# Kernel optimization log

Hardware: AMD Instinct MI355X
Metric: run time of the kernel (lower is better)

## Reference

```python
import jax, jax.numpy as jnp
import numpy as np

NUM_LAYERS = 2
D = 1024          # d_model
H = 16            # nhead
HD = D // H       # head_dim = 64
FF = 4096         # dim_feedforward
S, N, L = 1024, 2, 4096
EPS = 1e-5


def _layer_norm(x, g, b):
    mu = jnp.mean(x, axis=-1, keepdims=True)
    var = jnp.var(x, axis=-1, keepdims=True)
    return (x - mu) * jax.lax.rsqrt(var + EPS) * g + b


def setup_inputs() -> dict:
    key = jax.random.key(0)
    ks = jax.random.split(key, 16)
    w = 0.02
    return {
        "key_in": jax.random.normal(ks[0], (S, N, D), jnp.float32),
        "value_in": jax.random.normal(ks[1], (S, N, D), jnp.float32),
        "query": jax.random.normal(ks[2], (L, N, D), jnp.float32),
        "in_proj_w": jax.random.normal(ks[3], (NUM_LAYERS, 3 * D, D), jnp.float32) * w,
        "in_proj_b": jnp.zeros((NUM_LAYERS, 3 * D), jnp.float32),
        "out_w": jax.random.normal(ks[4], (NUM_LAYERS, D, D), jnp.float32) * w,
        "out_b": jnp.zeros((NUM_LAYERS, D), jnp.float32),
        "ln1_g": jnp.ones((NUM_LAYERS, D), jnp.float32),
        "ln1_b": jnp.zeros((NUM_LAYERS, D), jnp.float32),
        "ln2_g": jnp.ones((NUM_LAYERS, D), jnp.float32),
        "ln2_b": jnp.zeros((NUM_LAYERS, D), jnp.float32),
        "ff1_w": jax.random.normal(ks[5], (NUM_LAYERS, FF, D), jnp.float32) * w,
        "ff1_b": jnp.zeros((NUM_LAYERS, FF), jnp.float32),
        "ff2_w": jax.random.normal(ks[6], (NUM_LAYERS, D, FF), jnp.float32) * w,
        "ff2_b": jnp.zeros((NUM_LAYERS, D), jnp.float32),
    }


def reference(key_in, value_in, query, in_proj_w, in_proj_b, out_w, out_b,
              ln1_g, ln1_b, ln2_g, ln2_b, ff1_w, ff1_b, ff2_w, ff2_b):
    scaling = float(HD) ** -0.5
    noise_key = jax.random.key(42)
    tgt = query
    attn_map = None
    for i in range(NUM_LAYERS):
        Wq, Wk, Wv = in_proj_w[i, :D], in_proj_w[i, D:2 * D], in_proj_w[i, 2 * D:]
        bq, bk, bv = in_proj_b[i, :D], in_proj_b[i, D:2 * D], in_proj_b[i, 2 * D:]
        q = (tgt @ Wq.T + bq) * scaling              # [L,N,D]
        k = key_in @ Wk.T + bk                       # [S,N,D]
        v = value_in @ Wv.T + bv                     # [S,N,D]
        qh = q.reshape(L, N, H, HD).transpose(1, 2, 0, 3)   # [N,H,L,HD]
        kh = k.reshape(S, N, H, HD).transpose(1, 2, 0, 3)   # [N,H,S,HD]
        vh = v.reshape(S, N, H, HD).transpose(1, 2, 0, 3)   # [N,H,S,HD]
        scores = jnp.einsum('nhld,nhsd->nhls', qh, kh)      # [N,H,L,S]
        # add_noise_term: zero logit column + random value token
        scores = jnp.concatenate(
            [scores, jnp.zeros((N, H, L, 1), scores.dtype)], axis=-1)
        noise = jax.random.normal(jax.random.fold_in(noise_key, i),
                                  (N, H, 1, HD), vh.dtype)
        vh = jnp.concatenate([vh, noise], axis=2)           # [N,H,S+1,HD]
        w = jax.nn.softmax(scores, axis=-1)                 # [N,H,L,S+1]
        seg = jax.nn.sigmoid(w)                             # sigmoid of softmax
        out = jnp.einsum('nhls,nhsd->nhld', w, vh)          # [N,H,L,HD]
        out = out.transpose(2, 0, 1, 3).reshape(L, N, D)
        out = out @ out_w[i].T + out_b[i]
        attn_map = seg.mean(axis=1)[:, :, :-1]              # [N,L,S], noise col dropped
        x = _layer_norm(tgt + out, ln1_g[i], ln1_b[i])
        h = jax.nn.relu(x @ ff1_w[i].T + ff1_b[i]) @ ff2_w[i].T + ff2_b[i]
        tgt = _layer_norm(x + h, ln2_g[i], ln2_b[i])
    return tgt, attn_map
```

## Files before the change

kernel.cpp:

```cpp
#include <hip/hip_runtime.h>
#include <hip/hip_bf16.h>


typedef __bf16 bf16x8 __attribute__((ext_vector_type(8)));
typedef float  f32x4  __attribute__((ext_vector_type(4)));

__device__ __forceinline__ f32x4 mfma16(bf16x8 a, bf16x8 b, f32x4 c) {
    return __builtin_amdgcn_mfma_f32_16x16x32_bf16(a, b, c, 0, 0, 0);
}

__device__ __forceinline__ void load_lds16(const __bf16* g, __bf16* l) {
    __builtin_amdgcn_global_load_lds(
        (const __attribute__((address_space(1))) void*)g,
        (__attribute__((address_space(3))) void*)l, 16, 0, 0);
}

__device__ __forceinline__ int swz8(int o, int nwg) {
    return (o & 7) * (nwg >> 3) + (o >> 3);
}

__global__ __launch_bounds__(256) void cast_k(const float* __restrict__ in,
                                              __bf16* __restrict__ out, int n4) {
    int i = blockIdx.x * 256 + threadIdx.x;
    if (i >= n4) return;
    float4 f = ((const float4*)in)[i];
    union { uint2 u; __bf16 h[4]; } ob;
    ob.h[0] = (__bf16)f.x; ob.h[1] = (__bf16)f.y;
    ob.h[2] = (__bf16)f.z; ob.h[3] = (__bf16)f.w;
    ((uint2*)out)[i] = ob.u;
}

__global__ __launch_bounds__(512, 2) void gemm8p(
    const __bf16* __restrict__ A, const __bf16* __restrict__ B,
    const float* __restrict__ bias, __bf16* __restrict__ C,
    int N, int K, float scale, int relu)
{
    __shared__ __bf16 L[8][8192];
    const int tid = threadIdx.x;
    const int wid = tid >> 6, lane = tid & 63;
    const int lq = lane >> 4, lc = lane & 15;
    const int wm = wid >> 2;
    const int wn = (wid & 3) * 64;
    const int bh = wn >> 7;
    const int lb = wn & 127;
    const int sw = lc & 7;
    const int w = swz8(blockIdx.x, gridDim.x);
    const int nt = N >> 8;
    const int bm = (w / nt) * 256, bn = (w % nt) * 256;
    const int NT = K >> 6;

    auto stageA = [&](int kt, int h) {
#pragma unroll
        for (int p = 0; p < 2; ++p) {
            const int cc = p * 512 + tid;
            const int row = cc >> 3, gk = ((cc & 7) ^ (row & 7)) * 8;
            load_lds16(A + (size_t)(bm + h * 128 + row) * K + (kt * 64 + gk),
                       &L[(kt & 1) * 4 + h][(size_t)cc * 8]);
        }
    };
    auto stageB = [&](int kt, int h) {
#pragma unroll
        for (int p = 0; p < 2; ++p) {
            const int cc = p * 512 + tid;
            const int row = cc >> 3, gk = ((cc & 7) ^ (row & 7)) * 8;
            load_lds16(B + (size_t)(bn + h * 128 + row) * K + (kt * 64 + gk),
                       &L[(kt & 1) * 4 + 2 + h][(size_t)cc * 8]);
        }
    };

    stageA(0, 0); stageA(0, 1); stageB(0, 0); stageB(0, 1);
    stageA(1, 0); stageA(1, 1); stageB(1, 0); stageB(1, 1);
    asm volatile("s_waitcnt vmcnt(8)" ::: "memory");
    __builtin_amdgcn_s_barrier();
    __builtin_amdgcn_sched_barrier(0);

    const f32x4 fz = {0.f, 0.f, 0.f, 0.f};
    f32x4 acc[2][4][4];
#pragma unroll
    for (int rh = 0; rh < 2; ++rh)
#pragma unroll
        for (int i = 0; i < 4; ++i)
#pragma unroll
            for (int jj = 0; jj < 4; ++jj) acc[rh][i][jj] = fz;

    for (int t = 0; t < NT; ++t) {
        const __bf16* __restrict__ Ah = &L[(t & 1) * 4 + wm][0];
        const __bf16* __restrict__ Bh = &L[(t & 1) * 4 + 2 + bh][0];
        const int pf = (t + 2 < NT);
        bf16x8 a[2][4], b0[2][2], b1[2][2];

#pragma unroll
        for (int kk = 0; kk < 2; ++kk) {
            const int sl = ((kk * 4 + lq) ^ sw) * 8;
#pragma unroll
            for (int i = 0; i < 4; ++i)
                a[kk][i] = *(const bf16x8*)&Ah[(i * 16 + lc) * 64 + sl];
#pragma unroll
            for (int j = 0; j < 2; ++j)
                b0[kk][j] = *(const bf16x8*)&Bh[(lb + j * 16 + lc) * 64 + sl];
        }
        __builtin_amdgcn_s_barrier();
        asm volatile("s_waitcnt lgkmcnt(0)" ::: "memory");
        __builtin_amdgcn_sched_barrier(0);
        __builtin_amdgcn_s_setprio(1);
#pragma unroll
        for (int kk = 0; kk < 2; ++kk)
#pragma unroll
            for (int i = 0; i < 4; ++i)
#pragma unroll
                for (int j = 0; j < 2; ++j)
                    acc[0][i][j] = mfma16(a[kk][i], b0[kk][j], acc[0][i][j]);
        __builtin_amdgcn_s_setprio(0);
        __builtin_amdgcn_s_barrier();
        __builtin_amdgcn_sched_barrier(0);

#pragma unroll
        for (int kk = 0; kk < 2; ++kk) {
            const int sl = ((kk * 4 + lq) ^ sw) * 8;
#pragma unroll
            for (int j = 0; j < 2; ++j)
                b1[kk][j] = *(const bf16x8*)&Bh[(lb + 32 + j * 16 + lc) * 64 + sl];
        }
        __builtin_amdgcn_s_barrier();
        asm volatile("s_waitcnt lgkmcnt(0)" ::: "memory");
        __builtin_amdgcn_sched_barrier(0);
        __builtin_amdgcn_s_setprio(1);
#pragma unroll
        for (int kk = 0; kk < 2; ++kk)
#pragma unroll
            for (int i = 0; i < 4; ++i)
#pragma unroll
                for (int j = 0; j < 2; ++j)
                    acc[0][i][2 + j] = mfma16(a[kk][i], b1[kk][j], acc[0][i][2 + j]);
        __builtin_amdgcn_s_setprio(0);
        __builtin_amdgcn_s_barrier();
        __builtin_amdgcn_sched_barrier(0);

#pragma unroll
        for (int kk = 0; kk < 2; ++kk) {
            const int sl = ((kk * 4 + lq) ^ sw) * 8;
#pragma unroll
            for (int i = 0; i < 4; ++i)
                a[kk][i] = *(const bf16x8*)&Ah[(64 + i * 16 + lc) * 64 + sl];
        }
        if (pf) { stageB(t + 2, 0); stageB(t + 2, 1); }
        __builtin_amdgcn_s_barrier();
        asm volatile("s_waitcnt lgkmcnt(0)" ::: "memory");
        __builtin_amdgcn_sched_barrier(0);
        __builtin_amdgcn_s_setprio(1);
#pragma unroll
        for (int kk = 0; kk < 2; ++kk)
#pragma unroll
            for (int i = 0; i < 4; ++i)
#pragma unroll
                for (int j = 0; j < 2; ++j)
                    acc[1][i][j] = mfma16(a[kk][i], b0[kk][j], acc[1][i][j]);
        __builtin_amdgcn_s_setprio(0);
        __builtin_amdgcn_s_barrier();
        __builtin_amdgcn_sched_barrier(0);

        if (pf) { stageA(t + 2, 0); stageA(t + 2, 1); }
        __builtin_amdgcn_s_barrier();
        __builtin_amdgcn_sched_barrier(0);
        __builtin_amdgcn_s_setprio(1);
#pragma unroll
        for (int kk = 0; kk < 2; ++kk)
#pragma unroll
            for (int i = 0; i < 4; ++i)
#pragma unroll
                for (int j = 0; j < 2; ++j)
                    acc[1][i][2 + j] = mfma16(a[kk][i], b1[kk][j], acc[1][i][2 + j]);
        __builtin_amdgcn_s_setprio(0);
        if (pf) asm volatile("s_waitcnt vmcnt(8)" ::: "memory");
        else    asm volatile("s_waitcnt vmcnt(0)" ::: "memory");
        __builtin_amdgcn_s_barrier();
        __builtin_amdgcn_sched_barrier(0);
    }

    float bv[4];
#pragma unroll
    for (int q = 0; q < 4; ++q) bv[q] = bias[bn + wn + q * 16 + lc];
#pragma unroll
    for (int rh = 0; rh < 2; ++rh)
#pragma unroll
        for (int i = 0; i < 4; ++i)
#pragma unroll
            for (int r = 0; r < 4; ++r) {
                const int row = bm + wm * 128 + rh * 64 + i * 16 + lq * 4 + r;
                const size_t base = (size_t)row * N + bn + wn + lc;
#pragma unroll
                for (int ch = 0; ch < 2; ++ch)
#pragma unroll
                    for (int j = 0; j < 2; ++j) {
                        float v = (acc[rh][i][ch * 2 + j][r] + bv[ch * 2 + j]) * scale;
                        if (relu) v = fmaxf(v, 0.f);
                        C[base + ch * 32 + j * 16] = (__bf16)v;
                    }
            }
}

__global__ __launch_bounds__(512, 2) void gemm8pN(
    const __bf16* __restrict__ A, const __bf16* __restrict__ B,
    const float* __restrict__ bias, __bf16* __restrict__ C,
    int N, int K, float scale, int relu)
{
    __shared__ __bf16 L[6][8192];
    const int tid = threadIdx.x;
    const int wid = tid >> 6, lane = tid & 63;
    const int lq = lane >> 4, lc = lane & 15;
    const int wr = (wid >> 1) * 64;
    const int wc = (wid & 1) * 64;
    const int ha = wr >> 7;
    const int lr = wr & 127;
    const int sw = lc & 7;
    const int w = swz8(blockIdx.x, gridDim.x);
    const int nt = N >> 7;
    const int bm = (w / nt) * 256, bn = (w % nt) * 128;
    const int NT = K >> 6;

    auto stageA = [&](int kt, int h) {
#pragma unroll
        for (int p = 0; p < 2; ++p) {
            const int cc = p * 512 + tid;
            const int row = cc >> 3, gk = ((cc & 7) ^ (row & 7)) * 8;
            load_lds16(A + (size_t)(bm + h * 128 + row) * K + (kt * 64 + gk),
                       &L[(kt & 1) * 3 + h][(size_t)cc * 8]);
        }
    };
    auto stageB = [&](int kt) {
#pragma unroll
        for (int p = 0; p < 2; ++p) {
            const int cc = p * 512 + tid;
            const int row = cc >> 3, gk = ((cc & 7) ^ (row & 7)) * 8;
            load_lds16(B + (size_t)(bn + row) * K + (kt * 64 + gk),
                       &L[(kt & 1) * 3 + 2][(size_t)cc * 8]);
        }
    };

    stageA(0, 0); stageA(0, 1); stageB(0);
    stageA(1, 0); stageA(1, 1); stageB(1);
    asm volatile("s_waitcnt vmcnt(6)" ::: "memory");
    __builtin_amdgcn_s_barrier();
    __builtin_amdgcn_sched_barrier(0);

    const f32x4 fz = {0.f, 0.f, 0.f, 0.f};
    f32x4 acc[4][4];
#pragma unroll
    for (int i = 0; i < 4; ++i)
#pragma unroll
        for (int j = 0; j < 4; ++j) acc[i][j] = fz;

    for (int t = 0; t < NT; ++t) {
        const __bf16* __restrict__ Ah = &L[(t & 1) * 3 + ha][0];
        const __bf16* __restrict__ Bb = &L[(t & 1) * 3 + 2][0];
        const int pf = (t + 2 < NT);
        bf16x8 a[2][4], b[2][4];

#pragma unroll
        for (int kk = 0; kk < 2; ++kk) {
            const int sl = ((kk * 4 + lq) ^ sw) * 8;
#pragma unroll
            for (int i = 0; i < 4; ++i)
                a[kk][i] = *(const bf16x8*)&Ah[(lr + i * 16 + lc) * 64 + sl];
#pragma unroll
            for (int j = 0; j < 4; ++j)
                b[kk][j] = *(const bf16x8*)&Bb[(wc + j * 16 + lc) * 64 + sl];
        }
        __builtin_amdgcn_s_barrier();
        asm volatile("s_waitcnt lgkmcnt(0)" ::: "memory");
        __builtin_amdgcn_sched_barrier(0);
        __builtin_amdgcn_s_setprio(1);
#pragma unroll
        for (int i = 0; i < 4; ++i)
#pragma unroll
            for (int j = 0; j < 4; ++j)
                acc[i][j] = mfma16(a[0][i], b[0][j], acc[i][j]);
        __builtin_amdgcn_s_setprio(0);
        __builtin_amdgcn_s_barrier();
        __builtin_amdgcn_sched_barrier(0);

        if (pf) { stageB(t + 2); stageA(t + 2, 0); stageA(t + 2, 1); }
        __builtin_amdgcn_s_setprio(1);
#pragma unroll
        for (int i = 0; i < 4; ++i)
#pragma unroll
            for (int j = 0; j < 4; ++j)
                acc[i][j] = mfma16(a[1][i], b[1][j], acc[i][j]);
        __builtin_amdgcn_s_setprio(0);
        if (pf) asm volatile("s_waitcnt vmcnt(6)" ::: "memory");
        else    asm volatile("s_waitcnt vmcnt(0)" ::: "memory");
        __builtin_amdgcn_s_barrier();
        __builtin_amdgcn_sched_barrier(0);
    }

    float bv[4];
#pragma unroll
    for (int q = 0; q < 4; ++q) bv[q] = bias[bn + wc + q * 16 + lc];
#pragma unroll
    for (int i = 0; i < 4; ++i)
#pragma unroll
        for (int r = 0; r < 4; ++r) {
            const int row = bm + wr + i * 16 + lq * 4 + r;
            const size_t base = (size_t)row * N + bn + wc + lc;
#pragma unroll
            for (int j = 0; j < 4; ++j) {
                float v = (acc[i][j][r] + bv[j]) * scale;
                if (relu) v = fmaxf(v, 0.f);
                C[base + j * 16] = (__bf16)v;
            }
        }
}

template <int BN>
__device__ __forceinline__ void gemm_core(
    const __bf16* __restrict__ A, const __bf16* __restrict__ B,
    const float* __restrict__ bias, __bf16* __restrict__ C,
    int M, int N, int K, float scale, int relu, int bm, int bn,
    __bf16* As, __bf16* Bs)
{
    const int tid = threadIdx.x;
    const int wave = tid >> 6, lane = tid & 63;
    const int lq = lane >> 4, lc = lane & 15;
    const int WN = BN / 2;
    const int JT = WN / 16;
    const int wm = (wave >> 1) * 64, wn = (wave & 1) * WN;

    const f32x4 fz = {0.f, 0.f, 0.f, 0.f};
    f32x4 acc[4][4];
#pragma unroll
    for (int i = 0; i < 4; ++i)
#pragma unroll
        for (int j = 0; j < JT; ++j) acc[i][j] = fz;

    const int sw = lc & 7;

    for (int k0 = 0; k0 < K; k0 += 64) {
        __syncthreads();
#pragma unroll
        for (int i = 0; i < 4; ++i) {
            const int c = tid + 256 * i;
            const int row = c >> 3, gk = ((c & 7) ^ (row & 7)) * 8;
            load_lds16(A + (size_t)(bm + row) * K + (k0 + gk),
                       As + (size_t)c * 8);
        }
#pragma unroll
        for (int i = 0; i < BN / 32; ++i) {
            const int c = tid + 256 * i;
            const int row = c >> 3, gk = ((c & 7) ^ (row & 7)) * 8;
            load_lds16(B + (size_t)(bn + row) * K + (k0 + gk),
                       Bs + (size_t)c * 8);
        }
        __syncthreads();
#pragma unroll
        for (int kk = 0; kk < 2; ++kk) {
            bf16x8 af[4], bw[4];
            const int slot = ((kk * 4 + lq) ^ sw) * 8;
#pragma unroll
            for (int i = 0; i < 4; ++i)
                af[i] = *(const bf16x8*)&As[(wm + i * 16 + lc) * 64 + slot];
#pragma unroll
            for (int j = 0; j < JT; ++j)
                bw[j] = *(const bf16x8*)&Bs[(wn + j * 16 + lc) * 64 + slot];
#pragma unroll
            for (int i = 0; i < 4; ++i)
#pragma unroll
                for (int j = 0; j < JT; ++j)
                    acc[i][j] = mfma16(af[i], bw[j], acc[i][j]);
        }
    }

#pragma unroll
    for (int j = 0; j < JT; ++j) {
        const int col = bn + wn + j * 16 + lc;
        const float bv = bias[col];
#pragma unroll
        for (int i = 0; i < 4; ++i) {
#pragma unroll
            for (int r = 0; r < 4; ++r) {
                float v = (acc[i][j][r] + bv) * scale;
                if (relu) v = fmaxf(v, 0.f);
                const int row = bm + wm + i * 16 + lq * 4 + r;
                C[(size_t)row * N + col] = (__bf16)v;
            }
        }
    }
}

__global__ __launch_bounds__(256) void gemm_qkv(
    const __bf16* __restrict__ TGT, const __bf16* __restrict__ KIN,
    const __bf16* __restrict__ VIN, const __bf16* __restrict__ W,
    const float* __restrict__ bias, __bf16* __restrict__ PROJ,
    __bf16* __restrict__ KB, __bf16* __restrict__ VB)
{
    __shared__ __bf16 As[128 * 64];
    __shared__ __bf16 Bs[64 * 64];
    const int bid = swz8(blockIdx.x, 1536);
    const __bf16* A; __bf16* Cout; int M, t, seg; float scale;
    if (bid < 1024)      { seg = 0; t = bid;        A = TGT; Cout = PROJ; M = 8192; scale = 0.125f; }
    else if (bid < 1280) { seg = 1; t = bid - 1024; A = KIN; Cout = KB;   M = 2048; scale = 1.f; }
    else                 { seg = 2; t = bid - 1280; A = VIN; Cout = VB;   M = 2048; scale = 1.f; }
    gemm_core<64>(A, W + (size_t)seg * 1048576, bias + seg * 1024, Cout,
                  M, 1024, 1024, scale, 0, (t >> 4) * 128, (t & 15) * 64, As, Bs);
}

__global__ __launch_bounds__(256) void transpose_v(const __bf16* __restrict__ v,
                                                   __bf16* __restrict__ vt) {
    __shared__ __bf16 t[64][72];
    const int tid = threadIdx.x;
    const int s0 = blockIdx.x * 64, h = blockIdx.y, n = blockIdx.z;
#pragma unroll
    for (int i = 0; i < 2; ++i) {
        const int cc = tid + 256 * i, row = cc >> 3, kc = (cc & 7) * 8;
        *(uint4*)&t[row][kc] =
            *(const uint4*)(v + ((size_t)((s0 + row) * 2 + n)) * 1024 + h * 64 + kc);
    }
    __syncthreads();
#pragma unroll
    for (int i = 0; i < 2; ++i) {
        const int cc = tid + 256 * i, d = cc >> 3, jc = (cc & 7) * 8;
        __attribute__((aligned(16))) __bf16 tmp[8];
#pragma unroll
        for (int u = 0; u < 8; ++u) tmp[u] = t[jc + u][d];
        *(uint4*)(vt + ((size_t)((n * 16 + h) * 64 + d)) * 1024 + s0 + jc) = *(uint4*)tmp;
    }
}

__global__ __launch_bounds__(256) void attn_fused(
    const __bf16* __restrict__ q, const __bf16* __restrict__ kk,
    const __bf16* __restrict__ vt, float* __restrict__ cvec,
    __bf16* __restrict__ aout)
{
    __shared__ __bf16 qs[64][72];
    __shared__ __bf16 ks[64][72];
    __shared__ __bf16 vs[64][72];
    __shared__ __bf16 es[64][72];
    const int tid = threadIdx.x, wave = tid >> 6, lane = tid & 63;
    const int lq = lane >> 4, lc = lane & 15;
    const int o = (blockIdx.z * 16 + blockIdx.y) * 64 + blockIdx.x;
    const int w = swz8(o, 2048);
    const int l0 = (w & 63) * 64, h = (w >> 6) & 15, n = w >> 10;
    const int wr = wave * 16;
#pragma unroll
    for (int i = 0; i < 2; ++i) {
        const int cc = tid + 256 * i, row = cc >> 3, kc = (cc & 7) * 8;
        *(uint4*)&qs[row][kc] =
            *(const uint4*)(q + ((size_t)((l0 + row) * 2 + n)) * 1024 + h * 64 + kc);
    }
    const f32x4 fz = {0.f, 0.f, 0.f, 0.f};
    f32x4 oacc[4];
#pragma unroll
    for (int dj = 0; dj < 4; ++dj) oacc[dj] = fz;
    float den[4] = {0.f, 0.f, 0.f, 0.f};

    for (int st = 0; st < 16; ++st) {
        __syncthreads();
#pragma unroll
        for (int i = 0; i < 2; ++i) {
            const int cc = tid + 256 * i, row = cc >> 3, kc = (cc & 7) * 8;
            *(uint4*)&ks[row][kc] =
                *(const uint4*)(kk + ((size_t)((st * 64 + row) * 2 + n)) * 1024 + h * 64 + kc);
            *(uint4*)&vs[row][kc] =
                *(const uint4*)(vt + ((size_t)((n * 16 + h) * 64 + row)) * 1024 + st * 64 + kc);
        }
        __syncthreads();
        const bf16x8 a0 = *(const bf16x8*)&qs[wr + lc][lq * 8];
        const bf16x8 a1 = *(const bf16x8*)&qs[wr + lc][32 + lq * 8];
#pragma unroll
        for (int sj = 0; sj < 4; ++sj) {
            f32x4 acc = fz;
            const bf16x8 b0 = *(const bf16x8*)&ks[sj * 16 + lc][lq * 8];
            const bf16x8 b1 = *(const bf16x8*)&ks[sj * 16 + lc][32 + lq * 8];
            acc = mfma16(a0, b0, acc);
            acc = mfma16(a1, b1, acc);
#pragma unroll
            for (int r = 0; r < 4; ++r) {
                const float e = __expf(acc[r]);
                den[r] += e;
                es[wr + lq * 4 + r][sj * 16 + lc] = (__bf16)e;
            }
        }
        const bf16x8 w0 = *(const bf16x8*)&es[wr + lc][lq * 8];
        const bf16x8 w1 = *(const bf16x8*)&es[wr + lc][32 + lq * 8];
#pragma unroll
        for (int dj = 0; dj < 4; ++dj) {
            const bf16x8 v0 = *(const bf16x8*)&vs[dj * 16 + lc][lq * 8];
            const bf16x8 v1 = *(const bf16x8*)&vs[dj * 16 + lc][32 + lq * 8];
            oacc[dj] = mfma16(w0, v0, oacc[dj]);
            oacc[dj] = mfma16(w1, v1, oacc[dj]);
        }
    }
#pragma unroll
    for (int m = 1; m < 16; m <<= 1)
#pragma unroll
        for (int r = 0; r < 4; ++r) den[r] += __shfl_xor(den[r], m);
    float c_r[4];
#pragma unroll
    for (int r = 0; r < 4; ++r) c_r[r] = 1.f / (den[r] + 1.f);
    if (lc == 0) {
#pragma unroll
        for (int r = 0; r < 4; ++r)
            cvec[((size_t)(n * 16 + h)) * 4096 + (l0 + wr + lq * 4 + r)] = c_r[r];
    }
#pragma unroll
    for (int r = 0; r < 4; ++r) {
        const int l = l0 + wr + lq * 4 + r;
        const size_t base = ((size_t)l * 2 + n) * 1024 + h * 64 + lc;
#pragma unroll
        for (int dj = 0; dj < 4; ++dj)
            aout[base + dj * 16] = (__bf16)(oacc[dj][r] * c_r[r]);
    }
}

__global__ __launch_bounds__(256) void attn_map_k(
    const __bf16* __restrict__ q, const __bf16* __restrict__ kk,
    const float* __restrict__ cvec, float* __restrict__ amap)
{
    __shared__ __bf16 qs[64][72];
    __shared__ __bf16 ks[64][72];
    const int tid = threadIdx.x, wave = tid >> 6, lane = tid & 63;
    const int lq = lane >> 4, lc = lane & 15;
    const int o = (blockIdx.z * 16 + blockIdx.y) * 64 + blockIdx.x;
    const int w = swz8(o, 2048);
    const int l0 = (w & 63) * 64, st = (w >> 6) & 15, n = w >> 10;
    const int wr = wave * 16;
    float sig[4][4];
#pragma unroll
    for (int sj = 0; sj < 4; ++sj)
#pragma unroll
        for (int r = 0; r < 4; ++r) sig[sj][r] = 0.f;

    for (int h = 0; h < 16; ++h) {
        __syncthreads();
#pragma unroll
        for (int i = 0; i < 2; ++i) {
            const int cc = tid + 256 * i, row = cc >> 3, kc = (cc & 7) * 8;
            *(uint4*)&qs[row][kc] =
                *(const uint4*)(q + ((size_t)((l0 + row) * 2 + n)) * 1024 + h * 64 + kc);
            *(uint4*)&ks[row][kc] =
                *(const uint4*)(kk + ((size_t)((st * 64 + row) * 2 + n)) * 1024 + h * 64 + kc);
        }
        __syncthreads();
        float c_r[4];
#pragma unroll
        for (int r = 0; r < 4; ++r)
            c_r[r] = cvec[((size_t)(n * 16 + h)) * 4096 + (l0 + wr + lq * 4 + r)];
        const bf16x8 a0 = *(const bf16x8*)&qs[wr + lc][lq * 8];
        const bf16x8 a1 = *(const bf16x8*)&qs[wr + lc][32 + lq * 8];
#pragma unroll
        for (int sj = 0; sj < 4; ++sj) {
            const f32x4 fz = {0.f, 0.f, 0.f, 0.f};
            f32x4 acc = fz;
            const bf16x8 b0 = *(const bf16x8*)&ks[sj * 16 + lc][lq * 8];
            const bf16x8 b1 = *(const bf16x8*)&ks[sj * 16 + lc][32 + lq * 8];
            acc = mfma16(a0, b0, acc);
            acc = mfma16(a1, b1, acc);
#pragma unroll
            for (int r = 0; r < 4; ++r) {
                const float ww = __expf(acc[r]) * c_r[r];
                const float w2 = ww * ww;
                sig[sj][r] += 0.5f + ww * (0.25f - w2 * (1.f / 48.f - w2 * (1.f / 480.f)));
            }
        }
    }
#pragma unroll
    for (int r = 0; r < 4; ++r) {
        const int l = l0 + wr + lq * 4 + r;
        const size_t base = ((size_t)n * 4096 + l) * 1024 + st * 64 + lc;
#pragma unroll
        for (int sj = 0; sj < 4; ++sj)
            amap[base + sj * 16] = sig[sj][r] * (1.f / 16.f);
    }
}

__global__ __launch_bounds__(256) void ln_k(
    const float* __restrict__ basef, const __bf16* __restrict__ baseb,
    const __bf16* __restrict__ add,
    const float* __restrict__ g, const float* __restrict__ bb,
    float* __restrict__ out_f32, __bf16* __restrict__ out_bf)
{
    __shared__ float red[8];
    const int row = blockIdx.x, tid = threadIdx.x;
    const int col = tid * 4;
    const size_t off = (size_t)row * 1024 + col;
    float v[4];
    if (basef) {
        float4 t = *(const float4*)(basef + off);
        v[0] = t.x; v[1] = t.y; v[2] = t.z; v[3] = t.w;
    } else {
        union { uint2 u; __bf16 h[4]; } tb;
        tb.u = *(const uint2*)(baseb + off);
#pragma unroll
        for (int j = 0; j < 4; ++j) v[j] = (float)tb.h[j];
    }
    {
        union { uint2 u; __bf16 h[4]; } ub;
        ub.u = *(const uint2*)(add + off);
#pragma unroll
        for (int j = 0; j < 4; ++j) v[j] += (float)ub.h[j];
    }
    float s = v[0] + v[1] + v[2] + v[3];
    float q = v[0] * v[0] + v[1] * v[1] + v[2] * v[2] + v[3] * v[3];
#pragma unroll
    for (int m = 1; m < 64; m <<= 1) { s += __shfl_xor(s, m); q += __shfl_xor(q, m); }
    const int wave = tid >> 6, lane = tid & 63;
    if (lane == 0) { red[wave] = s; red[4 + wave] = q; }
    __syncthreads();
    s = red[0] + red[1] + red[2] + red[3];
    q = red[4] + red[5] + red[6] + red[7];
    const float mu = s * (1.f / 1024.f);
    const float var = q * (1.f / 1024.f) - mu * mu;
    const float rs = rsqrtf(var + 1e-5f);
    const float4 gv = *(const float4*)(g + col);
    const float4 bv = *(const float4*)(bb + col);
    float y[4];
    y[0] = (v[0] - mu) * rs * gv.x + bv.x;
    y[1] = (v[1] - mu) * rs * gv.y + bv.y;
    y[2] = (v[2] - mu) * rs * gv.z + bv.z;
    y[3] = (v[3] - mu) * rs * gv.w + bv.w;
    if (out_f32) {
        float4 o; o.x = y[0]; o.y = y[1]; o.z = y[2]; o.w = y[3];
        *(float4*)(out_f32 + off) = o;
    }
    if (out_bf) {
        union { uint2 u; __bf16 h[4]; } ob;
#pragma unroll
        for (int j = 0; j < 4; ++j) ob.h[j] = (__bf16)y[j];
        *(uint2*)(out_bf + off) = ob.u;
    }
}

extern "C" void kernel_launch(void* const* d_in, const int* in_sizes, int n_in,
                              void* d_out, int out_size, void* d_ws, size_t ws_size,
                              hipStream_t stream) {
    const float* key_in    = (const float*)d_in[0];
    const float* value_in  = (const float*)d_in[1];
    const float* query     = (const float*)d_in[2];
    const float* in_proj_w = (const float*)d_in[3];
    const float* in_proj_b = (const float*)d_in[4];
    const float* out_w     = (const float*)d_in[5];
    const float* out_b     = (const float*)d_in[6];
    const float* ln1_g     = (const float*)d_in[7];
    const float* ln1_b     = (const float*)d_in[8];
    const float* ln2_g     = (const float*)d_in[9];
    const float* ln2_b     = (const float*)d_in[10];
    const float* ff1_w     = (const float*)d_in[11];
    const float* ff1_b     = (const float*)d_in[12];
    const float* ff2_w     = (const float*)d_in[13];
    const float* ff2_b     = (const float*)d_in[14];
    float* outp = (float*)d_out;

    __bf16* ws = (__bf16*)d_ws;
    const size_t M1 = 1048576;
    __bf16* WQKV = ws;
    __bf16* WOUT = ws + 6 * M1;
    __bf16* WF1  = ws + 8 * M1;
    __bf16* WF2  = ws + 16 * M1;
    __bf16* KIN  = ws + 24 * M1;
    __bf16* VIN  = ws + 26 * M1;
    __bf16* TGT  = ws + 28 * M1;
    __bf16* PROJ = ws + 36 * M1;
    __bf16* KB   = ws + 44 * M1;
    __bf16* VB   = ws + 46 * M1;
    __bf16* VT   = ws + 48 * M1;
    __bf16* AOUT = ws + 50 * M1;
    __bf16* XB   = ws + 58 * M1;
    __bf16* H1   = ws + 66 * M1;
    float*  CVEC = (float*)(ws + 98 * M1);

    cast_k<<<8192, 256, 0, stream>>>(query, TGT, 2097152);
    cast_k<<<2048, 256, 0, stream>>>(key_in, KIN, 524288);
    cast_k<<<2048, 256, 0, stream>>>(value_in, VIN, 524288);
    cast_k<<<6144, 256, 0, stream>>>(in_proj_w, WQKV, 1572864);
    cast_k<<<2048, 256, 0, stream>>>(out_w, WOUT, 524288);
    cast_k<<<8192, 256, 0, stream>>>(ff1_w, WF1, 2097152);
    cast_k<<<8192, 256, 0, stream>>>(ff2_w, WF2, 2097152);

    for (int i = 0; i < 2; ++i) {
        __bf16* WQKVi = WQKV + (size_t)i * 3 * M1;
        __bf16* WOUTi = WOUT + (size_t)i * M1;
        __bf16* WF1i  = WF1 + (size_t)i * 4 * M1;
        __bf16* WF2i  = WF2 + (size_t)i * 4 * M1;

        gemm_qkv<<<1536, 256, 0, stream>>>(TGT, KIN, VIN, WQKVi,
                                           in_proj_b + i * 3072, PROJ, KB, VB);
        transpose_v<<<dim3(16, 16, 2), 256, 0, stream>>>(VB, VT);

        attn_fused<<<dim3(64, 16, 2), 256, 0, stream>>>(PROJ, KB, VT, CVEC, AOUT);
        if (i == 1)
            attn_map_k<<<dim3(64, 16, 2), 256, 0, stream>>>(PROJ, KB, CVEC,
                                                            outp + 8388608);

        gemm8pN<<<256, 512, 0, stream>>>(AOUT, WOUTi, out_b + i * 1024,
                                         PROJ, 1024, 1024, 1.f, 0);
        ln_k<<<8192, 256, 0, stream>>>(i == 0 ? query : nullptr,
                                       i == 0 ? nullptr : TGT,
                                       PROJ, ln1_g + i * 1024, ln1_b + i * 1024,
                                       nullptr, XB);
        gemm8p<<<512, 512, 0, stream>>>(XB, WF1i, ff1_b + i * 4096,
                                        H1, 4096, 1024, 1.f, 1);
        gemm8pN<<<256, 512, 0, stream>>>(H1, WF2i, ff2_b + i * 1024,
                                         AOUT, 1024, 4096, 1.f, 0);
        ln_k<<<8192, 256, 0, stream>>>(nullptr, XB, AOUT,
                                       ln2_g + i * 1024, ln2_b + i * 1024,
                                       i == 1 ? outp : nullptr, TGT);
    }
}
```

Before: 884.8 us.

## Use direct global-to-LDS loads with XOR swizzle and register-resident Q in attention kernels

Both attention kernels now load K and V tiles with global_load_lds straight into unpadded, XOR-swizzled shared-memory tiles instead of staging them through registers. The Q fragments are read from global memory into registers per lane rather than through a shared-memory tile. The softmax weight tile also uses the swizzled layout. This is meant to cut LDS footprint, bank conflicts and load instruction overhead. The trade-off is uncoalesced per-lane Q reads from global memory, and the loads are still unpipelined with no double buffering.

```diff
diff --git a/kernel.cpp b/kernel.cpp
--- a/kernel.cpp
+++ b/kernel.cpp
@@ -430,22 +430,23 @@
     const __bf16* __restrict__ vt, float* __restrict__ cvec,
     __bf16* __restrict__ aout)
 {
-    __shared__ __bf16 qs[64][72];
-    __shared__ __bf16 ks[64][72];
-    __shared__ __bf16 vs[64][72];
-    __shared__ __bf16 es[64][72];
+    __shared__ __bf16 ks[64 * 64];
+    __shared__ __bf16 vs[64 * 64];
+    __shared__ __bf16 es[64 * 64];
     const int tid = threadIdx.x, wave = tid >> 6, lane = tid & 63;
     const int lq = lane >> 4, lc = lane & 15;
     const int o = (blockIdx.z * 16 + blockIdx.y) * 64 + blockIdx.x;
     const int w = swz8(o, 2048);
     const int l0 = (w & 63) * 64, h = (w >> 6) & 15, n = w >> 10;
     const int wr = wave * 16;
-#pragma unroll
-    for (int i = 0; i < 2; ++i) {
-        const int cc = tid + 256 * i, row = cc >> 3, kc = (cc & 7) * 8;
-        *(uint4*)&qs[row][kc] =
-            *(const uint4*)(q + ((size_t)((l0 + row) * 2 + n)) * 1024 + h * 64 + kc);
-    }
+    const int sw = lc & 7;
+
+    bf16x8 aq[2];
+#pragma unroll
+    for (int k2 = 0; k2 < 2; ++k2)
+        aq[k2] = *(const bf16x8*)(q + ((size_t)((l0 + wr + lc) * 2 + n)) * 1024
+                                  + h * 64 + k2 * 32 + lq * 8);
+
     const f32x4 fz = {0.f, 0.f, 0.f, 0.f};
     f32x4 oacc[4];
 #pragma unroll
@@ -456,37 +457,44 @@
         __syncthreads();
 #pragma unroll
         for (int i = 0; i < 2; ++i) {
-            const int cc = tid + 256 * i, row = cc >> 3, kc = (cc & 7) * 8;
-            *(uint4*)&ks[row][kc] =
-                *(const uint4*)(kk + ((size_t)((st * 64 + row) * 2 + n)) * 1024 + h * 64 + kc);
-            *(uint4*)&vs[row][kc] =
-                *(const uint4*)(vt + ((size_t)((n * 16 + h) * 64 + row)) * 1024 + st * 64 + kc);
+            const int cc = tid + 256 * i;
+            const int row = cc >> 3, gk = ((cc & 7) ^ (row & 7)) * 8;
+            load_lds16(kk + ((size_t)((st * 64 + row) * 2 + n)) * 1024 + h * 64 + gk,
+                       ks + (size_t)cc * 8);
+            load_lds16(vt + ((size_t)((n * 16 + h) * 64 + row)) * 1024 + st * 64 + gk,
+                       vs + (size_t)cc * 8);
         }
         __syncthreads();
-        const bf16x8 a0 = *(const bf16x8*)&qs[wr + lc][lq * 8];
-        const bf16x8 a1 = *(const bf16x8*)&qs[wr + lc][32 + lq * 8];
 #pragma unroll
         for (int sj = 0; sj < 4; ++sj) {
             f32x4 acc = fz;
-            const bf16x8 b0 = *(const bf16x8*)&ks[sj * 16 + lc][lq * 8];
-            const bf16x8 b1 = *(const bf16x8*)&ks[sj * 16 + lc][32 + lq * 8];
-            acc = mfma16(a0, b0, acc);
-            acc = mfma16(a1, b1, acc);
+#pragma unroll
+            for (int k2 = 0; k2 < 2; ++k2) {
+                const bf16x8 b =
+                    *(const bf16x8*)&ks[(sj * 16 + lc) * 64 + ((k2 * 4 + lq) ^ sw) * 8];
+                acc = mfma16(aq[k2], b, acc);
+            }
 #pragma unroll
             for (int r = 0; r < 4; ++r) {
                 const float e = __expf(acc[r]);
                 den[r] += e;
-                es[wr + lq * 4 + r][sj * 16 + lc] = (__bf16)e;
+                const int R = wr + lq * 4 + r;
+                es[R * 64 + (((sj * 2 + (lc >> 3)) ^ (R & 7)) * 8) + (lc & 7)] =
+                    (__bf16)e;
             }
         }
-        const bf16x8 w0 = *(const bf16x8*)&es[wr + lc][lq * 8];
-        const bf16x8 w1 = *(const bf16x8*)&es[wr + lc][32 + lq * 8];
+        bf16x8 wv[2];
+#pragma unroll
+        for (int k2 = 0; k2 < 2; ++k2)
+            wv[k2] = *(const bf16x8*)&es[(wr + lc) * 64 + ((k2 * 4 + lq) ^ sw) * 8];
 #pragma unroll
         for (int dj = 0; dj < 4; ++dj) {
-            const bf16x8 v0 = *(const bf16x8*)&vs[dj * 16 + lc][lq * 8];
-            const bf16x8 v1 = *(const bf16x8*)&vs[dj * 16 + lc][32 + lq * 8];
-            oacc[dj] = mfma16(w0, v0, oacc[dj]);
-            oacc[dj] = mfma16(w1, v1, oacc[dj]);
+#pragma unroll
+            for (int k2 = 0; k2 < 2; ++k2) {
+                const bf16x8 vv =
+                    *(const bf16x8*)&vs[(dj * 16 + lc) * 64 + ((k2 * 4 + lq) ^ sw) * 8];
+                oacc[dj] = mfma16(wv[k2], vv, oacc[dj]);
+            }
         }
     }
 #pragma unroll
@@ -515,14 +523,14 @@
     const __bf16* __restrict__ q, const __bf16* __restrict__ kk,
     const float* __restrict__ cvec, float* __restrict__ amap)
 {
-    __shared__ __bf16 qs[64][72];
-    __shared__ __bf16 ks[64][72];
+    __shared__ __bf16 ks[64 * 64];
     const int tid = threadIdx.x, wave = tid >> 6, lane = tid & 63;
     const int lq = lane >> 4, lc = lane & 15;
     const int o = (blockIdx.z * 16 + blockIdx.y) * 64 + blockIdx.x;
     const int w = swz8(o, 2048);
     const int l0 = (w & 63) * 64, st = (w >> 6) & 15, n = w >> 10;
     const int wr = wave * 16;
+    const int sw = lc & 7;
     float sig[4][4];
 #pragma unroll
     for (int sj = 0; sj < 4; ++sj)
@@ -533,27 +541,31 @@
         __syncthreads();
 #pragma unroll
         for (int i = 0; i < 2; ++i) {
-            const int cc = tid + 256 * i, row = cc >> 3, kc = (cc & 7) * 8;
-            *(uint4*)&qs[row][kc] =
-                *(const uint4*)(q + ((size_t)((l0 + row) * 2 + n)) * 1024 + h * 64 + kc);
-            *(uint4*)&ks[row][kc] =
-                *(const uint4*)(kk + ((size_t)((st * 64 + row) * 2 + n)) * 1024 + h * 64 + kc);
+            const int cc = tid + 256 * i;
+            const int row = cc >> 3, gk = ((cc & 7) ^ (row & 7)) * 8;
+            load_lds16(kk + ((size_t)((st * 64 + row) * 2 + n)) * 1024 + h * 64 + gk,
+                       ks + (size_t)cc * 8);
         }
         __syncthreads();
         float c_r[4];
 #pragma unroll
         for (int r = 0; r < 4; ++r)
             c_r[r] = cvec[((size_t)(n * 16 + h)) * 4096 + (l0 + wr + lq * 4 + r)];
-        const bf16x8 a0 = *(const bf16x8*)&qs[wr + lc][lq * 8];
-        const bf16x8 a1 = *(const bf16x8*)&qs[wr + lc][32 + lq * 8];
+        bf16x8 aq[2];
+#pragma unroll
+        for (int k2 = 0; k2 < 2; ++k2)
+            aq[k2] = *(const bf16x8*)(q + ((size_t)((l0 + wr + lc) * 2 + n)) * 1024
+                                      + h * 64 + k2 * 32 + lq * 8);
 #pragma unroll
         for (int sj = 0; sj < 4; ++sj) {
             const f32x4 fz = {0.f, 0.f, 0.f, 0.f};
             f32x4 acc = fz;
-            const bf16x8 b0 = *(const bf16x8*)&ks[sj * 16 + lc][lq * 8];
-            const bf16x8 b1 = *(const bf16x8*)&ks[sj * 16 + lc][32 + lq * 8];
-            acc = mfma16(a0, b0, acc);
-            acc = mfma16(a1, b1, acc);
+#pragma unroll
+            for (int k2 = 0; k2 < 2; ++k2) {
+                const bf16x8 b =
+                    *(const bf16x8*)&ks[(sj * 16 + lc) * 64 + ((k2 * 4 + lq) ^ sw) * 8];
+                acc = mfma16(aq[k2], b, acc);
+            }
 #pragma unroll
             for (int r = 0; r < 4; ++r) {
                 const float ww = __expf(acc[r]) * c_r[r];
```

Result: faster. 854.8 us (-3.4%).
